# Kernel optimization log

Hardware: AMD Instinct MI355X
Metric: run time of the kernel (lower is better)

Reference implementation:

```python
import jax, jax.numpy as jnp
import numpy as np

M, A, H, T = 6, 4096, 128, 30   # num_modes, num_actors, hidden_size, future_steps
HIST = 50
MAX_T = 6.0
DT = MAX_T / T                   # min_stepsize: one Euler step per prediction interval
MIN_SCALE = 0.001
EPS = 1e-5

def _ln(x, g, b):
    mu = x.mean(-1, keepdims=True)
    v = ((x - mu) ** 2).mean(-1, keepdims=True)
    return (x - mu) * jax.lax.rsqrt(v + EPS) * g + b

def setup_inputs() -> dict:
    key = jax.random.key(0)
    ks = iter(jax.random.split(key, 64))
    def p(shape):
        return jax.random.normal(next(ks), shape, jnp.float32) * 0.02
    inp = {
        'local_embed':  jax.random.normal(next(ks), (A, H), jnp.float32),
        'global_embed': jax.random.normal(next(ks), (M, A, H), jnp.float32),
        'noise':        jax.random.normal(next(ks), (T, M * A, H), jnp.float32),
        # aggr_embed: Linear(2H,H) + LayerNorm
        'aggr_w': p((2 * H, H)), 'aggr_b': p((H,)),
        'aggr_g': jnp.ones((H,), jnp.float32), 'aggr_be': jnp.zeros((H,), jnp.float32),
        # FFunc (posterior drift): Linear(H+2,H)-Tanh-Linear(H,H)-Tanh-Linear(H,H)
        'f_w1': p((H + 2, H)), 'f_b1': p((H,)),
        'f_w2': p((H, H)),     'f_b2': p((H,)),
        'f_w3': p((H, H)),     'f_b3': p((H,)),
        # GFunc (diffusion): Linear(H+2,H)-Tanh-Linear(H,H)-Tanh-Linear(H,1)-Sigmoid
        'g_w1': p((H + 2, H)), 'g_b1': p((H,)),
        'g_w2': p((H, H)),     'g_b2': p((H,)),
        'g_w3': p((H, 1)),     'g_b3': p((1,)),
        # decoder: Linear(H,H)+LN+ReLU+Linear(H,2)
        'd_w1': p((H, H)), 'd_b1': p((H,)),
        'd_g': jnp.ones((H,), jnp.float32), 'd_be': jnp.zeros((H,), jnp.float32),
        'd_w2': p((H, 2)), 'd_b2': p((2,)),
        # scale head (uncertain=True): same structure as decoder
        's_w1': p((H, H)), 's_b1': p((H,)),
        's_g': jnp.ones((H,), jnp.float32), 's_be': jnp.zeros((H,), jnp.float32),
        's_w2': p((H, 2)), 's_b2': p((2,)),
        # pi head: Linear(2H,H)+LN+ReLU+Linear(H,1)
        'p_w1': p((2 * H, H)), 'p_b1': p((H,)),
        'p_g': jnp.ones((H,), jnp.float32), 'p_be': jnp.zeros((H,), jnp.float32),
        'p_w2': p((H, 1)), 'p_b2': p((1,)),
        'padding_mask': jnp.zeros((A, HIST), dtype=bool),
    }
    return inp

def reference(local_embed, global_embed, noise,
              aggr_w, aggr_b, aggr_g, aggr_be,
              f_w1, f_b1, f_w2, f_b2, f_w3, f_b3,
              g_w1, g_b1, g_w2, g_b2, g_w3, g_b3,
              d_w1, d_b1, d_g, d_be, d_w2, d_b2,
              s_w1, s_b1, s_g, s_be, s_w2, s_b2,
              p_w1, p_b1, p_g, p_be, p_w2, p_b2,
              padding_mask):
    N = M * A
    le = jnp.broadcast_to(local_embed, (M, A, H))
    # aggr_embed(cat(global, local))
    x = jnp.concatenate([global_embed, le], axis=-1)
    h0 = jax.nn.relu(_ln(x @ aggr_w + aggr_b, aggr_g, aggr_be)).reshape(N, H)

    def with_time(y, t):
        tc = jnp.ones((y.shape[0], 1), y.dtype) * t
        return jnp.concatenate([y, jnp.sin(tc), jnp.cos(tc)], axis=-1)

    def drift(t, y):  # FFunc
        i = with_time(y, t)
        h = jnp.tanh(i @ f_w1 + f_b1)
        h = jnp.tanh(h @ f_w2 + f_b2)
        return h @ f_w3 + f_b3

    def diffusion(t, y):  # GFunc -> scalar per sample, repeated over dims
        i = with_time(y, t)
        h = jnp.tanh(i @ g_w1 + g_b1)
        h = jnp.tanh(h @ g_w2 + g_b2)
        return jax.nn.sigmoid(h @ g_w3 + g_b3)  # [N,1]

    ts = jnp.linspace(0.0, MAX_T, T + 1)[:-1]  # left endpoints of each Euler step
    sqdt = jnp.sqrt(jnp.asarray(DT, h0.dtype))

    def step(y, tz):
        t, z = tz
        y2 = y + drift(t, y) * DT + diffusion(t, y) * sqdt * z
        return y2, y2

    _, ys = jax.lax.scan(step, h0, (ts, noise))  # [T, N, H]
    sol_y = ys.transpose(1, 0, 2)                # [N, T, H]

    dh = jax.nn.relu(_ln(sol_y @ d_w1 + d_b1, d_g, d_be))
    loc = (dh @ d_w2 + d_b2).reshape(M, A, T, 2)
    sh = jax.nn.relu(_ln(sol_y @ s_w1 + s_b1, s_g, s_be))
    scale = jax.nn.elu(sh @ s_w2 + s_b2) + 1.0 + MIN_SCALE
    scale = scale.reshape(M, A, T, 2)
    loc_out = jnp.concatenate([loc, scale], axis=-1)  # [M, A, T, 4]

    pin = jnp.concatenate([le, global_embed], axis=-1)
    pi = (jax.nn.relu(_ln(pin @ p_w1 + p_b1, p_g, p_be)) @ p_w2 + p_b2)
    pi = pi.squeeze(-1).T                              # [A, M]

    reg_mask = ~padding_mask[:, -T:]
    return loc_out, pi, reg_mask
```

## Files before the change

kernel.cpp:

```cpp
#include <hip/hip_runtime.h>

#define Adim 4096
#define HD 128
#define TSTEPS 30
#define NROWS 24576
#define RBLK 32
#define NBLKS 768
#define DT_C 0.2f
#define SQDT_C 0.44721359549995794f
#define LN_EPS 1e-5f

#define PI_OFF   2949120
#define MASK_OFF 2973696

typedef unsigned short u16;
typedef __bf16 bf16x8 __attribute__((ext_vector_type(8)));
typedef float f32x4 __attribute__((ext_vector_type(4)));

__device__ __forceinline__ u16 f2bf(float x){
    unsigned u = __builtin_bit_cast(unsigned, x);
    u = (u + 0x7fffu + ((u >> 16) & 1u)) >> 16;
    return (u16)u;
}
__device__ __forceinline__ float bf2f(unsigned h){
    unsigned u = (h & 0xffffu) << 16;
    return __builtin_bit_cast(float, u);
}
__device__ __forceinline__ unsigned pack2(float a, float b){
    unsigned r;
    asm("v_cvt_pk_bf16_f32 %0, %1, %2" : "=v"(r) : "v"(a), "v"(b));
    return r;
}
__device__ __forceinline__ float tanh_f(float x){
    return 1.0f - 2.0f / (1.0f + __expf(2.0f * x));
}
__device__ __forceinline__ float sigm_f(float x){
    return 1.0f / (1.0f + __expf(-x));
}
#define SWZ(r,k) ((k) ^ (((r)&7)<<3))

#define MFMA(A,B,C) __builtin_amdgcn_mfma_f32_16x16x32_bf16(A, B, C, 0, 0, 0)

__device__ __forceinline__ void loadW(const u16* __restrict__ img, int lane, int wid,
                                      bf16x8 W[4]) {
    const int c = wid*16 + (lane & 15);
    const int kq = lane >> 4;
#pragma unroll
    for (int kk = 0; kk < 4; ++kk)
        W[kk] = *reinterpret_cast<const bf16x8*>(img + c*HD + SWZ(c, kk*32 + kq*8));
}

__device__ __forceinline__ void gemm1(const u16* __restrict__ act, const bf16x8 (&W)[4],
                                      int lane, f32x4 acc[2]) {
    const int rl = lane & 15, kq = lane >> 4;
#pragma unroll
    for (int tr = 0; tr < 2; ++tr) {
        const int r = tr*16 + rl;
        const u16* arow = act + r*HD;
        f32x4 a = {0.f,0.f,0.f,0.f};
#pragma unroll
        for (int kk = 0; kk < 4; ++kk) {
            bf16x8 bf = *reinterpret_cast<const bf16x8*>(arow + SWZ(r, kk*32 + kq*8));
            a = MFMA(W[kk], bf, a);
        }
        acc[tr] = a;
    }
}
__device__ __forceinline__ void gemm2(const u16* __restrict__ act,
                                      const bf16x8 (&Wx)[4], const bf16x8 (&Wy)[4],
                                      int lane, f32x4 accX[2], f32x4 accY[2]) {
    const int rl = lane & 15, kq = lane >> 4;
#pragma unroll
    for (int tr = 0; tr < 2; ++tr) {
        const int r = tr*16 + rl;
        const u16* arow = act + r*HD;
        f32x4 ax = {0.f,0.f,0.f,0.f}, ay = {0.f,0.f,0.f,0.f};
#pragma unroll
        for (int kk = 0; kk < 4; ++kk) {
            bf16x8 bf = *reinterpret_cast<const bf16x8*>(arow + SWZ(r, kk*32 + kq*8));
            ax = MFMA(Wx[kk], bf, ax);
            ay = MFMA(Wy[kk], bf, ay);
        }
        accX[tr] = ax; accY[tr] = ay;
    }
}
__device__ __forceinline__ void gemm4(const u16* __restrict__ act,
                                      const bf16x8 (&W1)[4], const bf16x8 (&W2)[4],
                                      const bf16x8 (&W3)[4], const bf16x8 (&W4)[4],
                                      int lane, f32x4 a1[2], f32x4 a2[2],
                                      f32x4 a3[2], f32x4 a4[2]) {
    const int rl = lane & 15, kq = lane >> 4;
#pragma unroll
    for (int tr = 0; tr < 2; ++tr) {
        const int r = tr*16 + rl;
        const u16* arow = act + r*HD;
        f32x4 x1={0.f,0.f,0.f,0.f}, x2={0.f,0.f,0.f,0.f};
        f32x4 x3={0.f,0.f,0.f,0.f}, x4={0.f,0.f,0.f,0.f};
#pragma unroll
        for (int kk = 0; kk < 4; ++kk) {
            bf16x8 bf = *reinterpret_cast<const bf16x8*>(arow + SWZ(r, kk*32 + kq*8));
            x1 = MFMA(W1[kk], bf, x1);
            x2 = MFMA(W2[kk], bf, x2);
            x3 = MFMA(W3[kk], bf, x3);
            x4 = MFMA(W4[kk], bf, x4);
        }
        a1[tr]=x1; a2[tr]=x2; a3[tr]=x3; a4[tr]=x4;
    }
}

__device__ __forceinline__ void epiT(const f32x4 acc[2], const float b[4],
                                     u16* dst, int lane, int wid) {
    const int c0 = wid*16 + ((lane>>4)<<2);
    const int rl = lane & 15;
#pragma unroll
    for (int tr = 0; tr < 2; ++tr) {
        int r = tr*16 + rl;
        float v0 = tanh_f(acc[tr][0] + b[0]);
        float v1 = tanh_f(acc[tr][1] + b[1]);
        float v2 = tanh_f(acc[tr][2] + b[2]);
        float v3 = tanh_f(acc[tr][3] + b[3]);
        uint2 pk = { pack2(v0, v1), pack2(v2, v3) };
        *reinterpret_cast<uint2*>(dst + r*HD + SWZ(r, c0)) = pk;
    }
}
__device__ __forceinline__ void epiN(const f32x4 acc[2], const float b[4],
                                     u16* dst, int lane, int wid) {
    const int c0 = wid*16 + ((lane>>4)<<2);
    const int rl = lane & 15;
#pragma unroll
    for (int tr = 0; tr < 2; ++tr) {
        int r = tr*16 + rl;
        uint2 pk = { pack2(acc[tr][0]+b[0], acc[tr][1]+b[1]),
                     pack2(acc[tr][2]+b[2], acc[tr][3]+b[3]) };
        *reinterpret_cast<uint2*>(dst + r*HD + SWZ(r, c0)) = pk;
    }
}
__device__ __forceinline__ void epiF(const f32x4 acc[2], const float* __restrict__ bias,
                                     float* dst, int lane, int wid) {
    const int c0 = wid*16 + ((lane>>4)<<2);
    const int rl = lane & 15;
    float4 b4 = *reinterpret_cast<const float4*>(bias + c0);
#pragma unroll
    for (int tr = 0; tr < 2; ++tr) {
        int r = tr*16 + rl;
        float4 v = { acc[tr][0]+b4.x, acc[tr][1]+b4.y, acc[tr][2]+b4.z, acc[tr][3]+b4.w };
        *reinterpret_cast<float4*>(dst + r*HD + c0) = v;
    }
}

__device__ __forceinline__ void gemmX(const u16* __restrict__ Xc, int kBase,
                                      const u16* __restrict__ img,
                                      int lane, int wid, f32x4 acc[2], bool init) {
    bf16x8 W[4]; loadW(img, lane, wid, W);
    const int rl = lane & 15, kq = lane >> 4;
#pragma unroll
    for (int tr = 0; tr < 2; ++tr) {
        const int r = tr*16 + rl;
        const u16* arow = Xc + r*256;
        f32x4 a = init ? f32x4{0.f,0.f,0.f,0.f} : acc[tr];
#pragma unroll
        for (int kk = 0; kk < 4; ++kk) {
            bf16x8 bf = *reinterpret_cast<const bf16x8*>(arow + SWZ(r, kBase + kk*32 + kq*8));
            a = MFMA(W[kk], bf, a);
        }
        acc[tr] = a;
    }
}

__device__ __forceinline__ void head_ln(const u16* __restrict__ src,
                                        const float4* __restrict__ pp4,
                                        float b20, float b21, int elu, int off, int idx,
                                        float* __restrict__ outStage)
{
    int row = idx >> 3, sub = idx & 7;
    int c0 = sub * 16;
    uint4 p0 = *reinterpret_cast<const uint4*>(src + row*HD + SWZ(row, c0));
    uint4 p1 = *reinterpret_cast<const uint4*>(src + row*HD + SWZ(row, c0+8));
    float v[16];
    v[0]=bf2f(p0.x); v[1]=bf2f(p0.x>>16); v[2]=bf2f(p0.y); v[3]=bf2f(p0.y>>16);
    v[4]=bf2f(p0.z); v[5]=bf2f(p0.z>>16); v[6]=bf2f(p0.w); v[7]=bf2f(p0.w>>16);
    v[8]=bf2f(p1.x); v[9]=bf2f(p1.x>>16); v[10]=bf2f(p1.y); v[11]=bf2f(p1.y>>16);
    v[12]=bf2f(p1.z); v[13]=bf2f(p1.z>>16); v[14]=bf2f(p1.w); v[15]=bf2f(p1.w>>16);
    float s = 0.f, sq = 0.f;
#pragma unroll
    for (int i = 0; i < 16; ++i){ s += v[i]; sq += v[i]*v[i]; }
    s += __shfl_xor(s,1); sq += __shfl_xor(sq,1);
    s += __shfl_xor(s,2); sq += __shfl_xor(sq,2);
    s += __shfl_xor(s,4); sq += __shfl_xor(sq,4);
    float mu = s * (1.f/128.f);
    float rstd = rsqrtf(sq*(1.f/128.f) - mu*mu + LN_EPS);
    float a0 = 0.f, a1 = 0.f;
#pragma unroll
    for (int i = 0; i < 16; ++i){
        float4 p = pp4[(c0 + i) ^ sub];
        float h = (v[i]-mu)*rstd*p.x + p.y;
        h = fmaxf(h, 0.f);
        a0 += h * p.z; a1 += h * p.w;
    }
    a0 += __shfl_xor(a0,1); a1 += __shfl_xor(a1,1);
    a0 += __shfl_xor(a0,2); a1 += __shfl_xor(a1,2);
    a0 += __shfl_xor(a0,4); a1 += __shfl_xor(a1,4);
    if (sub == 0){
        a0 += b20; a1 += b21;
        if (elu){
            a0 = (a0 > 0.f ? a0 : __expf(a0)-1.f) + 1.001f;
            a1 = (a1 > 0.f ? a1 : __expf(a1)-1.f) + 1.001f;
        }
        outStage[row*4 + off]   = a0;
        outStage[row*4 + off+1] = a1;
    }
}

__global__ void prep_w(const float* __restrict__ fw1, const float* __restrict__ fw2,
                       const float* __restrict__ fw3, const float* __restrict__ gw1,
                       const float* __restrict__ gw2, const float* __restrict__ dw1,
                       const float* __restrict__ sw1, const float* __restrict__ aw,
                       const float* __restrict__ pw1, u16* __restrict__ ws)
{
    int img = blockIdx.y;
    int idx = blockIdx.x * 256 + threadIdx.x;
    int k = idx >> 7, j = idx & 127;
    const float* W = fw1; int sr = k;
    switch (img) {
        case 0: W = fw1; break;  case 1: W = fw2; break;  case 2: W = fw3; break;
        case 3: W = gw1; break;  case 4: W = gw2; break;
        case 5: W = dw1; break;  case 6: W = sw1; break;
        case 7: W = aw;  break;  case 8: W = aw;  sr = k + 128; break;
        case 9: W = pw1; break;  case 10: W = pw1; sr = k + 128; break;
    }
    ws[(size_t)img*16384 + j*128 + SWZ(j, k)] = f2bf(W[(size_t)sr*128 + j]);
}

__global__ void reorder_out(const float* __restrict__ wsOut, float* __restrict__ outp)
{
    __shared__ float tile[3840];
    int b = blockIdx.x;
    const float* src = wsOut + (size_t)b*3840;
#pragma unroll
    for (int j = 0; j < 15; ++j) {
        int idx = j*256 + threadIdx.x;
        int tt = idx >> 7, rc = idx & 127;
        int row = rc >> 2, c = idx & 3;
        tile[row*120 + tt*4 + c] = src[idx];
    }
    __syncthreads();
    float* dst = outp + (size_t)b*3840;
#pragma unroll
    for (int j = 0; j < 15; ++j) {
        int idx = j*256 + threadIdx.x;
        dst[idx] = tile[idx];
    }
}

__global__ __launch_bounds__(512, 2) void sde_fused(
    const float* __restrict__ lE, const float* __restrict__ gE,
    const float* __restrict__ noise,
    const float* __restrict__ aggr_b, const float* __restrict__ aggr_g, const float* __restrict__ aggr_be,
    const float* __restrict__ fw1, const float* __restrict__ fb1,
    const float* __restrict__ fb2, const float* __restrict__ fb3,
    const float* __restrict__ gw1, const float* __restrict__ gb1,
    const float* __restrict__ gb2, const float* __restrict__ gw3, const float* __restrict__ gb3,
    const float* __restrict__ db1, const float* __restrict__ dg, const float* __restrict__ dbe,
    const float* __restrict__ dw2, const float* __restrict__ db2,
    const float* __restrict__ sb1, const float* __restrict__ sg, const float* __restrict__ sbe,
    const float* __restrict__ sw2, const float* __restrict__ sb2,
    const float* __restrict__ pb1, const float* __restrict__ pg, const float* __restrict__ pbe,
    const float* __restrict__ pw2, const float* __restrict__ pb2,
    const unsigned char* __restrict__ pmask,
    const u16* __restrict__ wimg,
    float* __restrict__ wsOut,
    float* __restrict__ outp)
{
    __shared__ __align__(16) unsigned char SMEM[61952];
    u16*  Sb    = (u16*)SMEM;
    u16*  Ab    = (u16*)(SMEM + 8192);
    u16*  Bb    = (u16*)(SMEM + 16384);
    u16*  Cb    = (u16*)(SMEM + 24576);
    u16*  Fb    = (u16*)(SMEM + 32768);
    u16*  Db    = (u16*)(SMEM + 40960);
    u16*  Eb    = (u16*)(SMEM + 49152);
    float4* ppd = (float4*)(SMEM + 57344);
    float4* pps = (float4*)(SMEM + 59392);
    float* outStage = (float*)(SMEM + 61440);
    u16*  Xc    = (u16*)(SMEM + 40960);
    float* preLN = (float*)(SMEM + 8192);

    const int tid  = threadIdx.x;
    const int lane = tid & 63;
    const int wid  = tid >> 6;
    const int bid  = blockIdx.x;
    const int r0   = bid * RBLK;
    const int c0e  = wid*16 + ((lane>>4)<<2);

    if (tid < 128) {
        int cs = tid ^ ((tid >> 4) & 7);
        ppd[cs] = make_float4(dg[tid], dbe[tid], dw2[2*tid], dw2[2*tid+1]);
        pps[cs] = make_float4(sg[tid], sbe[tid], sw2[2*tid], sw2[2*tid+1]);
    }
#pragma unroll
    for (int i = 0; i < 2; ++i) {
        int gidx = i*512 + tid;
        int r = gidx >> 5;
        int k = (gidx & 31) * 8;
        int gr = r0 + r;
        const float* src = (k < HD) ? (gE + (size_t)gr*HD + k)
                                    : (lE + (size_t)(gr & (Adim-1))*HD + (k - HD));
        float4 v0 = reinterpret_cast<const float4*>(src)[0];
        float4 v1 = reinterpret_cast<const float4*>(src)[1];
        uint4 pk = { pack2(v0.x, v0.y), pack2(v0.z, v0.w),
                     pack2(v1.x, v1.y), pack2(v1.z, v1.w) };
        *reinterpret_cast<uint4*>(Xc + r*256 + SWZ(r, k)) = pk;
    }
    __syncthreads();

    f32x4 acc[2];

    gemmX(Xc, 0,   wimg + 10*16384, lane, wid, acc, true);
    gemmX(Xc, 128, wimg + 9*16384,  lane, wid, acc, false);
    epiF(acc, pb1, preLN, lane, wid);
    __syncthreads();
    {
        int row = tid >> 4, sub = tid & 15;
        int c0 = sub * 8;
        const float* yr = preLN + row*HD + c0;
        float v[8]; float s = 0.f, sq = 0.f;
#pragma unroll
        for (int i = 0; i < 8; ++i){ float x = yr[i]; v[i] = x; s += x; sq += x*x; }
        s += __shfl_xor(s,1); sq += __shfl_xor(sq,1);
        s += __shfl_xor(s,2); sq += __shfl_xor(sq,2);
        s += __shfl_xor(s,4); sq += __shfl_xor(sq,4);
        s += __shfl_xor(s,8); sq += __shfl_xor(sq,8);
        float mu = s*(1.f/128.f);
        float rstd = rsqrtf(sq*(1.f/128.f) - mu*mu + LN_EPS);
        float a0 = 0.f;
#pragma unroll
        for (int i = 0; i < 8; ++i){
            int cc = c0 + i;
            float h = (v[i]-mu)*rstd*pg[cc] + pbe[cc];
            a0 += fmaxf(h, 0.f) * pw2[cc];
        }
        a0 += __shfl_xor(a0,1); a0 += __shfl_xor(a0,2);
        a0 += __shfl_xor(a0,4); a0 += __shfl_xor(a0,8);
        if (sub == 0) {
            int gr = r0 + row;
            outp[PI_OFF + (size_t)(gr & (Adim-1))*6 + (gr >> 12)] = a0 + pb2[0];
        }
    }
    if (tid < RBLK) {
        int gr = r0 + tid;
        if (gr < Adim) {
            const unsigned char* pm = pmask + (size_t)gr*50 + 20;
            float* o = outp + MASK_OFF + (size_t)gr*TSTEPS;
#pragma unroll
            for (int i = 0; i < TSTEPS; ++i) o[i] = pm[i] ? 0.f : 1.f;
        }
    }
    __syncthreads();

    gemmX(Xc, 0,   wimg + 7*16384, lane, wid, acc, true);
    gemmX(Xc, 128, wimg + 8*16384, lane, wid, acc, false);
    __syncthreads();
    epiF(acc, aggr_b, preLN, lane, wid);
    __syncthreads();

    float y0,y1,y2,y3,y4,y5,y6,y7;
    {
        int row = tid >> 4, sub = tid & 15;
        int c0 = sub * 8;
        const float* yr = preLN + row*HD + c0;
        float v[8]; float s = 0.f, sq = 0.f;
#pragma unroll
        for (int i = 0; i < 8; ++i){ float x = yr[i]; v[i] = x; s += x; sq += x*x; }
        s += __shfl_xor(s,1); sq += __shfl_xor(sq,1);
        s += __shfl_xor(s,2); sq += __shfl_xor(sq,2);
        s += __shfl_xor(s,4); sq += __shfl_xor(sq,4);
        s += __shfl_xor(s,8); sq += __shfl_xor(sq,8);
        float mu = s*(1.f/128.f);
        float rstd = rsqrtf(sq*(1.f/128.f) - mu*mu + LN_EPS);
#pragma unroll
        for (int i = 0; i < 8; ++i){
            int cc = c0 + i;
            float h = (v[i]-mu)*rstd*aggr_g[cc] + aggr_be[cc];
            v[i] = fmaxf(h, 0.f);
        }
        y0=v[0]; y1=v[1]; y2=v[2]; y3=v[3]; y4=v[4]; y5=v[5]; y6=v[6]; y7=v[7];
        uint4 pk = { pack2(v[0],v[1]), pack2(v[2],v[3]),
                     pack2(v[4],v[5]), pack2(v[6],v[7]) };
        *reinterpret_cast<uint4*>(&Sb[row*HD + SWZ(row, c0)]) = pk;
    }

    bf16x8 WF1[4], WG1[4], WF2[4], WG2[4], WF3[4], WD1[4], WS1[4];
    loadW(wimg + 0*16384, lane, wid, WF1);
    loadW(wimg + 3*16384, lane, wid, WG1);
    loadW(wimg + 1*16384, lane, wid, WF2);
    loadW(wimg + 4*16384, lane, wid, WG2);
    loadW(wimg + 2*16384, lane, wid, WF3);
    loadW(wimg + 5*16384, lane, wid, WD1);
    loadW(wimg + 6*16384, lane, wid, WS1);

    float fb2c[4], gb2c[4], fb3c[4], db1c[4], sb1c[4];
    float fb1c[4], gb1c[4], fw1s[4], fw1cc[4], gw1s[4], gw1cc[4];
#pragma unroll
    for (int q = 0; q < 4; ++q) {
        int c = c0e + q;
        fb2c[q]=fb2[c]; gb2c[q]=gb2[c]; fb3c[q]=fb3[c]; db1c[q]=db1[c]; sb1c[q]=sb1[c];
        fb1c[q]=fb1[c]; gb1c[q]=gb1[c];
        fw1s[q]=fw1[128*HD+c]; fw1cc[q]=fw1[129*HD+c];
        gw1s[q]=gw1[128*HD+c]; gw1cc[q]=gw1[129*HD+c];
    }
    float g3r[8];
#pragma unroll
    for (int j = 0; j < 8; ++j) g3r[j] = gw3[(tid & 15)*8 + j];
    const float db20 = db2[0], db21 = db2[1];
    const float sb20 = sb2[0], sb21 = sb2[1];
    const float gb3v = gb3[0];

    float4 nz0, nz1;
    __syncthreads();

    {
        float bF[4], bG[4];
#pragma unroll
        for (int q = 0; q < 4; ++q) { bF[q] = fb1c[q] + fw1cc[q]; bG[q] = gb1c[q] + gw1cc[q]; }
        f32x4 aF[2], aG[2];
        gemm2(Sb, WF1, WG1, lane, aF, aG);
        epiT(aF, bF, Ab, lane, wid);
        epiT(aG, bG, Bb, lane, wid);
        const float* np = noise + ((size_t)r0)*HD + (size_t)tid*8;
        nz0 = reinterpret_cast<const float4*>(np)[0];
        nz1 = reinterpret_cast<const float4*>(np)[1];
    }
    __syncthreads();

    for (int k = 0; k < TSTEPS; ++k) {
        {
            f32x4 a1[2];
            gemm1(Ab, WF2, lane, a1);
            epiT(a1, fb2c, Cb, lane, wid);
            gemm1(Bb, WG2, lane, a1);
            epiT(a1, gb2c, Fb, lane, wid);
        }
        if (k) {
            if (tid < 256) head_ln(Db, ppd, db20, db21, 0, 0, tid, outStage);
            else           head_ln(Eb, pps, sb20, sb21, 1, 2, tid-256, outStage);
        }
        __syncthreads();
        {
            f32x4 a1[2];
            gemm1(Cb, WF3, lane, a1);
            epiN(a1, fb3c, Db, lane, wid);
        }
        float growv;
        {
            int row = tid >> 4, sub = tid & 15;
            uint4 pk = *reinterpret_cast<const uint4*>(Fb + row*HD + SWZ(row, sub*8));
            float s = bf2f(pk.x)*g3r[0] + bf2f(pk.x>>16)*g3r[1]
                    + bf2f(pk.y)*g3r[2] + bf2f(pk.y>>16)*g3r[3]
                    + bf2f(pk.z)*g3r[4] + bf2f(pk.z>>16)*g3r[5]
                    + bf2f(pk.w)*g3r[6] + bf2f(pk.w>>16)*g3r[7];
            s += __shfl_xor(s,1); s += __shfl_xor(s,2);
            s += __shfl_xor(s,4); s += __shfl_xor(s,8);
            growv = sigm_f(s + gb3v);
        }
        __syncthreads();
        {
            int row = tid >> 4, sub = tid & 15;
            int sk = SWZ(row, sub*8);
            uint4 dpk = *reinterpret_cast<const uint4*>(Db + row*HD + sk);
            float g = growv * SQDT_C;
            y0 += bf2f(dpk.x)     * DT_C + g*nz0.x;
            y1 += bf2f(dpk.x>>16) * DT_C + g*nz0.y;
            y2 += bf2f(dpk.y)     * DT_C + g*nz0.z;
            y3 += bf2f(dpk.y>>16) * DT_C + g*nz0.w;
            y4 += bf2f(dpk.z)     * DT_C + g*nz1.x;
            y5 += bf2f(dpk.z>>16) * DT_C + g*nz1.y;
            y6 += bf2f(dpk.w)     * DT_C + g*nz1.z;
            y7 += bf2f(dpk.w>>16) * DT_C + g*nz1.w;
            uint4 s4 = { pack2(y0,y1), pack2(y2,y3), pack2(y4,y5), pack2(y6,y7) };
            *reinterpret_cast<uint4*>(Sb + row*HD + sk) = s4;
        }
        __syncthreads();
        if (k < TSTEPS-1) {
            float t = (k+1) * DT_C;
            float st = __sinf(t), ct = __cosf(t);
            float bF[4], bG[4];
#pragma unroll
            for (int q = 0; q < 4; ++q) {
                bF[q] = fb1c[q] + st*fw1s[q] + ct*fw1cc[q];
                bG[q] = gb1c[q] + st*gw1s[q] + ct*gw1cc[q];
            }
            f32x4 aF[2], aG[2], aD[2], aS[2];
            gemm4(Sb, WF1, WG1, WD1, WS1, lane, aF, aG, aD, aS);
            epiT(aF, bF, Ab, lane, wid);
            epiT(aG, bG, Bb, lane, wid);
            epiN(aD, db1c, Db, lane, wid);
            epiN(aS, sb1c, Eb, lane, wid);
            const float* np = noise + ((size_t)(k+1)*NROWS + r0)*HD + (size_t)tid*8;
            nz0 = reinterpret_cast<const float4*>(np)[0];
            nz1 = reinterpret_cast<const float4*>(np)[1];
            if (k >= 1 && tid < 128)
                wsOut[((size_t)bid*TSTEPS + (k-1))*128 + tid] = outStage[tid];
        } else {
            f32x4 aD[2], aS[2];
            gemm2(Sb, WD1, WS1, lane, aD, aS);
            epiN(aD, db1c, Db, lane, wid);
            epiN(aS, sb1c, Eb, lane, wid);
            if (tid < 128)
                wsOut[((size_t)bid*TSTEPS + (TSTEPS-2))*128 + tid] = outStage[tid];
        }
        __syncthreads();
    }
    if (tid < 256) head_ln(Db, ppd, db20, db21, 0, 0, tid, outStage);
    else           head_ln(Eb, pps, sb20, sb21, 1, 2, tid-256, outStage);
    __syncthreads();
    if (tid < 128)
        wsOut[((size_t)bid*TSTEPS + (TSTEPS-1))*128 + tid] = outStage[tid];
}

extern "C" void kernel_launch(void* const* d_in, const int* in_sizes, int n_in,
                              void* d_out, int out_size, void* d_ws, size_t ws_size,
                              hipStream_t stream) {
    const float* lE      = (const float*)d_in[0];
    const float* gE      = (const float*)d_in[1];
    const float* noise   = (const float*)d_in[2];
    const float* aggr_w  = (const float*)d_in[3];
    const float* aggr_b  = (const float*)d_in[4];
    const float* aggr_g  = (const float*)d_in[5];
    const float* aggr_be = (const float*)d_in[6];
    const float* fw1 = (const float*)d_in[7];
    const float* fb1 = (const float*)d_in[8];
    const float* fw2 = (const float*)d_in[9];
    const float* fb2 = (const float*)d_in[10];
    const float* fw3 = (const float*)d_in[11];
    const float* fb3 = (const float*)d_in[12];
    const float* gw1 = (const float*)d_in[13];
    const float* gb1 = (const float*)d_in[14];
    const float* gw2 = (const float*)d_in[15];
    const float* gb2 = (const float*)d_in[16];
    const float* gw3 = (const float*)d_in[17];
    const float* gb3 = (const float*)d_in[18];
    const float* dw1 = (const float*)d_in[19];
    const float* db1 = (const float*)d_in[20];
    const float* dg  = (const float*)d_in[21];
    const float* dbe = (const float*)d_in[22];
    const float* dw2 = (const float*)d_in[23];
    const float* db2 = (const float*)d_in[24];
    const float* sw1 = (const float*)d_in[25];
    const float* sb1 = (const float*)d_in[26];
    const float* sg  = (const float*)d_in[27];
    const float* sbe = (const float*)d_in[28];
    const float* sw2 = (const float*)d_in[29];
    const float* sb2 = (const float*)d_in[30];
    const float* pw1 = (const float*)d_in[31];
    const float* pb1 = (const float*)d_in[32];
    const float* pg  = (const float*)d_in[33];
    const float* pbe = (const float*)d_in[34];
    const float* pw2 = (const float*)d_in[35];
    const float* pb2 = (const float*)d_in[36];
    const unsigned char* pmask = (const unsigned char*)d_in[37];
    float* outp = (float*)d_out;
    u16* wimg = (u16*)d_ws;
    float* wsOut = (float*)((char*)d_ws + 360448);

    prep_w<<<dim3(64, 11), 256, 0, stream>>>(fw1, fw2, fw3, gw1, gw2, dw1, sw1,
                                             aggr_w, pw1, wimg);
    sde_fused<<<NBLKS, 512, 0, stream>>>(
        lE, gE, noise, aggr_b, aggr_g, aggr_be,
        fw1, fb1, fb2, fb3,
        gw1, gb1, gb2, gw3, gb3,
        db1, dg, dbe, dw2, db2,
        sb1, sg, sbe, sw2, sb2,
        pb1, pg, pbe, pw2, pb2,
        pmask, wimg, wsOut, outp);
    reorder_out<<<NBLKS, 256, 0, stream>>>(wsOut, outp);
}
```

Before: 593.5 us.

## Interleave three 32-row sub-tiles per block in a staggered phase pipeline

```diff
diff --git a/kernel.cpp b/kernel.cpp
--- a/kernel.cpp
+++ b/kernel.cpp
@@ -4,8 +4,8 @@
 #define HD 128
 #define TSTEPS 30
 #define NROWS 24576
-#define RBLK 32
-#define NBLKS 768
+#define RBLK 96
+#define NBLKS 256
 #define DT_C 0.2f
 #define SQDT_C 0.44721359549995794f
 #define LN_EPS 1e-5f
@@ -38,7 +38,6 @@
     return 1.0f / (1.0f + __expf(-x));
 }
 #define SWZ(r,k) ((k) ^ (((r)&7)<<3))
-
 #define MFMA(A,B,C) __builtin_amdgcn_mfma_f32_16x16x32_bf16(A, B, C, 0, 0, 0)
 
 __device__ __forceinline__ void loadW(const u16* __restrict__ img, int lane, int wid,
@@ -209,6 +208,228 @@
         outStage[row*4 + off]   = a0;
         outStage[row*4 + off+1] = a1;
     }
+}
+
+__device__ __forceinline__ void ph0x(int st, const u16* Sb, u16* Ab, u16* Bb,
+    u16* Db, u16* Eb, const float* biasT, int lane, int wid, int c0e,
+    const bf16x8 (&WF1)[4], const bf16x8 (&WG1)[4],
+    const bf16x8 (&WD1)[4], const bf16x8 (&WS1)[4])
+{
+    const bool doL1 = (st < TSTEPS), doDS = (st >= 1);
+    float bF[4], bG[4], bD[4], bS[4];
+    if (doL1) {
+        float tt = st * DT_C;
+        float sn = __sinf(tt), cn = __cosf(tt);
+        float4 a0 = *(const float4*)(biasT + 0*128 + c0e);
+        float4 a1 = *(const float4*)(biasT + 1*128 + c0e);
+        float4 a2 = *(const float4*)(biasT + 2*128 + c0e);
+        float4 a3 = *(const float4*)(biasT + 3*128 + c0e);
+        float4 a4 = *(const float4*)(biasT + 4*128 + c0e);
+        float4 a5 = *(const float4*)(biasT + 5*128 + c0e);
+#pragma unroll
+        for (int q = 0; q < 4; ++q) {
+            bF[q] = ((const float*)&a0)[q] + sn*((const float*)&a1)[q] + cn*((const float*)&a2)[q];
+            bG[q] = ((const float*)&a3)[q] + sn*((const float*)&a4)[q] + cn*((const float*)&a5)[q];
+        }
+    }
+    if (doDS) {
+        float4 a9 = *(const float4*)(biasT + 9*128 + c0e);
+        float4 aa = *(const float4*)(biasT + 10*128 + c0e);
+#pragma unroll
+        for (int q = 0; q < 4; ++q) { bD[q]=((const float*)&a9)[q]; bS[q]=((const float*)&aa)[q]; }
+    }
+    if (doL1 && doDS) {
+        f32x4 aF[2], aG[2], aD[2], aS[2];
+        gemm4(Sb, WF1, WG1, WD1, WS1, lane, aF, aG, aD, aS);
+        epiT(aF, bF, Ab, lane, wid);
+        epiT(aG, bG, Bb, lane, wid);
+        epiN(aD, bD, Db, lane, wid);
+        epiN(aS, bS, Eb, lane, wid);
+    } else if (doL1) {
+        f32x4 aF[2], aG[2];
+        gemm2(Sb, WF1, WG1, lane, aF, aG);
+        epiT(aF, bF, Ab, lane, wid);
+        epiT(aG, bG, Bb, lane, wid);
+    } else if (doDS) {
+        f32x4 aD[2], aS[2];
+        gemm2(Sb, WD1, WS1, lane, aD, aS);
+        epiN(aD, bD, Db, lane, wid);
+        epiN(aS, bS, Eb, lane, wid);
+    }
+}
+
+__device__ __forceinline__ void ph1x(int st, const u16* Ab, const u16* Bb, u16* Cb,
+    const u16* Db, const u16* Eb, float* gpw, float* outS,
+    const float4* ppd, const float4* pps, const float* biasT,
+    int tid, int lane, int wid, int c0e,
+    float db20, float db21, float sb20, float sb21,
+    const bf16x8 (&WF2)[4], const bf16x8 (&WG2)[4])
+{
+    if (st < TSTEPS) {
+        float4 b6 = *(const float4*)(biasT + 6*128 + c0e);
+        float bb[4] = { b6.x, b6.y, b6.z, b6.w };
+        f32x4 a1[2];
+        gemm1(Ab, WF2, lane, a1);
+        epiT(a1, bb, Cb, lane, wid);
+        float4 b7 = *(const float4*)(biasT + 7*128 + c0e);
+        float4 g3 = *(const float4*)(biasT + 11*128 + c0e);
+        gemm1(Bb, WG2, lane, a1);
+        float p0 = tanh_f(a1[0][0]+b7.x)*g3.x + tanh_f(a1[0][1]+b7.y)*g3.y
+                 + tanh_f(a1[0][2]+b7.z)*g3.z + tanh_f(a1[0][3]+b7.w)*g3.w;
+        float p1 = tanh_f(a1[1][0]+b7.x)*g3.x + tanh_f(a1[1][1]+b7.y)*g3.y
+                 + tanh_f(a1[1][2]+b7.z)*g3.z + tanh_f(a1[1][3]+b7.w)*g3.w;
+        p0 += __shfl_xor(p0, 16); p0 += __shfl_xor(p0, 32);
+        p1 += __shfl_xor(p1, 16); p1 += __shfl_xor(p1, 32);
+        if ((lane >> 4) == 0) {
+            int rl2 = lane & 15;
+            gpw[rl2*9 + wid]      = p0;
+            gpw[(16+rl2)*9 + wid] = p1;
+        }
+    }
+    if (st >= 1) {
+        if (tid < 256) head_ln(Db, ppd, db20, db21, 0, 0, tid, outS);
+        else           head_ln(Eb, pps, sb20, sb21, 1, 2, tid-256, outS);
+    }
+}
+
+__device__ __forceinline__ void ph2x(int st, const u16* Cb, u16* Db,
+    const float* gpr, const float* biasT, const float* __restrict__ nbase,
+    float* __restrict__ wsb, const float* outS,
+    int tid, int lane, int wid, int c0e, float gb3v,
+    float4& nz0, float4& nz1, float& grow, const bf16x8 (&WF3)[4])
+{
+    if (st < TSTEPS) {
+        const float* np = nbase + (size_t)st*NROWS*HD + (size_t)tid*8;
+        nz0 = reinterpret_cast<const float4*>(np)[0];
+        nz1 = reinterpret_cast<const float4*>(np)[1];
+        float4 b8 = *(const float4*)(biasT + 8*128 + c0e);
+        float bb[4] = { b8.x, b8.y, b8.z, b8.w };
+        f32x4 a1[2];
+        gemm1(Cb, WF3, lane, a1);
+        epiN(a1, bb, Db, lane, wid);
+        int row = tid >> 4, sub = tid & 15;
+        float s = (sub < 8) ? gpr[row*9 + sub] : 0.f;
+        s += __shfl_xor(s,1); s += __shfl_xor(s,2);
+        s += __shfl_xor(s,4); s += __shfl_xor(s,8);
+        grow = sigm_f(s + gb3v) * SQDT_C;
+    }
+    if (st >= 1 && tid < 128)
+        wsb[(size_t)(st-1)*128 + tid] = outS[tid];
+}
+
+__device__ __forceinline__ void ph3x(int st, const u16* Db, u16* Sb, int tid,
+    float (&y)[8], const float4& nz0, const float4& nz1, float grow)
+{
+    if (st >= TSTEPS) return;
+    int row = tid >> 4, k0 = (tid & 15)*8, sk = SWZ(row, k0);
+    uint4 dpk = *reinterpret_cast<const uint4*>(Db + row*HD + sk);
+    y[0] += bf2f(dpk.x)     * DT_C + grow*nz0.x;
+    y[1] += bf2f(dpk.x>>16) * DT_C + grow*nz0.y;
+    y[2] += bf2f(dpk.y)     * DT_C + grow*nz0.z;
+    y[3] += bf2f(dpk.y>>16) * DT_C + grow*nz0.w;
+    y[4] += bf2f(dpk.z)     * DT_C + grow*nz1.x;
+    y[5] += bf2f(dpk.z>>16) * DT_C + grow*nz1.y;
+    y[6] += bf2f(dpk.w)     * DT_C + grow*nz1.z;
+    y[7] += bf2f(dpk.w>>16) * DT_C + grow*nz1.w;
+    uint4 s4 = { pack2(y[0],y[1]), pack2(y[2],y[3]), pack2(y[4],y[5]), pack2(y[6],y[7]) };
+    *reinterpret_cast<uint4*>(Sb + row*HD + sk) = s4;
+}
+
+__device__ __forceinline__ void prologueB(int rb0, u16* Xc, float* preLN, u16* Sb,
+    const float* lE, const float* gE,
+    const float* aggr_b, const float* aggr_g, const float* aggr_be,
+    const float* pb1, const float* pg, const float* pbe,
+    const float* pw2, const float* pb2,
+    const unsigned char* pmask, const u16* wimg, float* outp,
+    int tid, int lane, int wid, float (&y)[8])
+{
+#pragma unroll
+    for (int i = 0; i < 2; ++i) {
+        int gidx = i*512 + tid;
+        int r = gidx >> 5;
+        int k = (gidx & 31) * 8;
+        int gr = rb0 + r;
+        const float* src = (k < HD) ? (gE + (size_t)gr*HD + k)
+                                    : (lE + (size_t)(gr & (Adim-1))*HD + (k - HD));
+        float4 v0 = reinterpret_cast<const float4*>(src)[0];
+        float4 v1 = reinterpret_cast<const float4*>(src)[1];
+        uint4 pk = { pack2(v0.x, v0.y), pack2(v0.z, v0.w),
+                     pack2(v1.x, v1.y), pack2(v1.z, v1.w) };
+        *reinterpret_cast<uint4*>(Xc + r*256 + SWZ(r, k)) = pk;
+    }
+    __syncthreads();
+    f32x4 acc[2];
+    gemmX(Xc, 0,   wimg + 10*16384, lane, wid, acc, true);
+    gemmX(Xc, 128, wimg + 9*16384,  lane, wid, acc, false);
+    epiF(acc, pb1, preLN, lane, wid);
+    __syncthreads();
+    {
+        int row = tid >> 4, sub = tid & 15;
+        int c0 = sub * 8;
+        const float* yr = preLN + row*HD + c0;
+        float v[8]; float s = 0.f, sq = 0.f;
+#pragma unroll
+        for (int i = 0; i < 8; ++i){ float x = yr[i]; v[i] = x; s += x; sq += x*x; }
+        s += __shfl_xor(s,1); sq += __shfl_xor(sq,1);
+        s += __shfl_xor(s,2); sq += __shfl_xor(sq,2);
+        s += __shfl_xor(s,4); sq += __shfl_xor(sq,4);
+        s += __shfl_xor(s,8); sq += __shfl_xor(sq,8);
+        float mu = s*(1.f/128.f);
+        float rstd = rsqrtf(sq*(1.f/128.f) - mu*mu + LN_EPS);
+        float a0 = 0.f;
+#pragma unroll
+        for (int i = 0; i < 8; ++i){
+            int cc = c0 + i;
+            float h = (v[i]-mu)*rstd*pg[cc] + pbe[cc];
+            a0 += fmaxf(h, 0.f) * pw2[cc];
+        }
+        a0 += __shfl_xor(a0,1); a0 += __shfl_xor(a0,2);
+        a0 += __shfl_xor(a0,4); a0 += __shfl_xor(a0,8);
+        if (sub == 0) {
+            int gr = rb0 + row;
+            outp[PI_OFF + (size_t)(gr & (Adim-1))*6 + (gr >> 12)] = a0 + pb2[0];
+        }
+    }
+    if (tid < 32) {
+        int gr = rb0 + tid;
+        if (gr < Adim) {
+            const unsigned char* pm = pmask + (size_t)gr*50 + 20;
+            float* o = outp + MASK_OFF + (size_t)gr*TSTEPS;
+#pragma unroll
+            for (int i = 0; i < TSTEPS; ++i) o[i] = pm[i] ? 0.f : 1.f;
+        }
+    }
+    __syncthreads();
+    gemmX(Xc, 0,   wimg + 7*16384, lane, wid, acc, true);
+    gemmX(Xc, 128, wimg + 8*16384, lane, wid, acc, false);
+    epiF(acc, aggr_b, preLN, lane, wid);
+    __syncthreads();
+    {
+        int row = tid >> 4, sub = tid & 15;
+        int c0 = sub * 8;
+        const float* yr = preLN + row*HD + c0;
+        float v[8]; float s = 0.f, sq = 0.f;
+#pragma unroll
+        for (int i = 0; i < 8; ++i){ float x = yr[i]; v[i] = x; s += x; sq += x*x; }
+        s += __shfl_xor(s,1); sq += __shfl_xor(sq,1);
+        s += __shfl_xor(s,2); sq += __shfl_xor(sq,2);
+        s += __shfl_xor(s,4); sq += __shfl_xor(sq,4);
+        s += __shfl_xor(s,8); sq += __shfl_xor(sq,8);
+        float mu = s*(1.f/128.f);
+        float rstd = rsqrtf(sq*(1.f/128.f) - mu*mu + LN_EPS);
+#pragma unroll
+        for (int i = 0; i < 8; ++i){
+            int cc = c0 + i;
+            float h = (v[i]-mu)*rstd*aggr_g[cc] + aggr_be[cc];
+            v[i] = fmaxf(h, 0.f);
+        }
+#pragma unroll
+        for (int i = 0; i < 8; ++i) y[i] = v[i];
+        uint4 pk = { pack2(v[0],v[1]), pack2(v[2],v[3]),
+                     pack2(v[4],v[5]), pack2(v[6],v[7]) };
+        *reinterpret_cast<uint4*>(&Sb[row*HD + SWZ(row, c0)]) = pk;
+    }
+    __syncthreads();
 }
 
 __global__ void prep_w(const float* __restrict__ fw1, const float* __restrict__ fw2,
@@ -271,19 +492,23 @@
     float* __restrict__ wsOut,
     float* __restrict__ outp)
 {
-    __shared__ __align__(16) unsigned char SMEM[61952];
-    u16*  Sb    = (u16*)SMEM;
-    u16*  Ab    = (u16*)(SMEM + 8192);
-    u16*  Bb    = (u16*)(SMEM + 16384);
-    u16*  Cb    = (u16*)(SMEM + 24576);
-    u16*  Fb    = (u16*)(SMEM + 32768);
-    u16*  Db    = (u16*)(SMEM + 40960);
-    u16*  Eb    = (u16*)(SMEM + 49152);
-    float4* ppd = (float4*)(SMEM + 57344);
-    float4* pps = (float4*)(SMEM + 59392);
-    float* outStage = (float*)(SMEM + 61440);
-    u16*  Xc    = (u16*)(SMEM + 40960);
-    float* preLN = (float*)(SMEM + 8192);
+    __shared__ __align__(16) unsigned char SMEM[161536];
+    u16* Sb0 = (u16*)(SMEM +      0); u16* Ab0 = (u16*)(SMEM +  8192);
+    u16* Bb0 = (u16*)(SMEM +  16384); u16* Cb0 = (u16*)(SMEM + 24576);
+    u16* Db0 = (u16*)(SMEM +  32768); u16* Eb0 = (u16*)(SMEM + 40960);
+    u16* Sb1 = (u16*)(SMEM +  49152); u16* Ab1 = (u16*)(SMEM + 57344);
+    u16* Bb1 = (u16*)(SMEM +  65536); u16* Cb1 = (u16*)(SMEM + 73728);
+    u16* Db1 = (u16*)(SMEM +  81920); u16* Eb1 = (u16*)(SMEM + 90112);
+    u16* Sb2 = (u16*)(SMEM +  98304); u16* Ab2 = (u16*)(SMEM + 106496);
+    u16* Bb2 = (u16*)(SMEM + 114688); u16* Cb2 = (u16*)(SMEM + 122880);
+    u16* Db2 = (u16*)(SMEM + 131072); u16* Eb2 = (u16*)(SMEM + 139264);
+    float* gpart = (float*)(SMEM + 147456);
+    float* biasT = (float*)(SMEM + 149760);
+    float4* ppd  = (float4*)(SMEM + 155904);
+    float4* pps  = (float4*)(SMEM + 157952);
+    float* outS0 = (float*)(SMEM + 160000);
+    float* outS1 = (float*)(SMEM + 160512);
+    float* outS2 = (float*)(SMEM + 161024);
 
     const int tid  = threadIdx.x;
     const int lane = tid & 63;
@@ -296,98 +521,27 @@
         int cs = tid ^ ((tid >> 4) & 7);
         ppd[cs] = make_float4(dg[tid], dbe[tid], dw2[2*tid], dw2[2*tid+1]);
         pps[cs] = make_float4(sg[tid], sbe[tid], sw2[2*tid], sw2[2*tid+1]);
-    }
-#pragma unroll
-    for (int i = 0; i < 2; ++i) {
-        int gidx = i*512 + tid;
-        int r = gidx >> 5;
-        int k = (gidx & 31) * 8;
-        int gr = r0 + r;
-        const float* src = (k < HD) ? (gE + (size_t)gr*HD + k)
-                                    : (lE + (size_t)(gr & (Adim-1))*HD + (k - HD));
-        float4 v0 = reinterpret_cast<const float4*>(src)[0];
-        float4 v1 = reinterpret_cast<const float4*>(src)[1];
-        uint4 pk = { pack2(v0.x, v0.y), pack2(v0.z, v0.w),
-                     pack2(v1.x, v1.y), pack2(v1.z, v1.w) };
-        *reinterpret_cast<uint4*>(Xc + r*256 + SWZ(r, k)) = pk;
-    }
-    __syncthreads();
-
-    f32x4 acc[2];
-
-    gemmX(Xc, 0,   wimg + 10*16384, lane, wid, acc, true);
-    gemmX(Xc, 128, wimg + 9*16384,  lane, wid, acc, false);
-    epiF(acc, pb1, preLN, lane, wid);
-    __syncthreads();
-    {
-        int row = tid >> 4, sub = tid & 15;
-        int c0 = sub * 8;
-        const float* yr = preLN + row*HD + c0;
-        float v[8]; float s = 0.f, sq = 0.f;
-#pragma unroll
-        for (int i = 0; i < 8; ++i){ float x = yr[i]; v[i] = x; s += x; sq += x*x; }
-        s += __shfl_xor(s,1); sq += __shfl_xor(sq,1);
-        s += __shfl_xor(s,2); sq += __shfl_xor(sq,2);
-        s += __shfl_xor(s,4); sq += __shfl_xor(sq,4);
-        s += __shfl_xor(s,8); sq += __shfl_xor(sq,8);
-        float mu = s*(1.f/128.f);
-        float rstd = rsqrtf(sq*(1.f/128.f) - mu*mu + LN_EPS);
-        float a0 = 0.f;
-#pragma unroll
-        for (int i = 0; i < 8; ++i){
-            int cc = c0 + i;
-            float h = (v[i]-mu)*rstd*pg[cc] + pbe[cc];
-            a0 += fmaxf(h, 0.f) * pw2[cc];
-        }
-        a0 += __shfl_xor(a0,1); a0 += __shfl_xor(a0,2);
-        a0 += __shfl_xor(a0,4); a0 += __shfl_xor(a0,8);
-        if (sub == 0) {
-            int gr = r0 + row;
-            outp[PI_OFF + (size_t)(gr & (Adim-1))*6 + (gr >> 12)] = a0 + pb2[0];
-        }
-    }
-    if (tid < RBLK) {
-        int gr = r0 + tid;
-        if (gr < Adim) {
-            const unsigned char* pm = pmask + (size_t)gr*50 + 20;
-            float* o = outp + MASK_OFF + (size_t)gr*TSTEPS;
-#pragma unroll
-            for (int i = 0; i < TSTEPS; ++i) o[i] = pm[i] ? 0.f : 1.f;
-        }
-    }
-    __syncthreads();
-
-    gemmX(Xc, 0,   wimg + 7*16384, lane, wid, acc, true);
-    gemmX(Xc, 128, wimg + 8*16384, lane, wid, acc, false);
-    __syncthreads();
-    epiF(acc, aggr_b, preLN, lane, wid);
-    __syncthreads();
-
-    float y0,y1,y2,y3,y4,y5,y6,y7;
-    {
-        int row = tid >> 4, sub = tid & 15;
-        int c0 = sub * 8;
-        const float* yr = preLN + row*HD + c0;
-        float v[8]; float s = 0.f, sq = 0.f;
-#pragma unroll
-        for (int i = 0; i < 8; ++i){ float x = yr[i]; v[i] = x; s += x; sq += x*x; }
-        s += __shfl_xor(s,1); sq += __shfl_xor(sq,1);
-        s += __shfl_xor(s,2); sq += __shfl_xor(sq,2);
-        s += __shfl_xor(s,4); sq += __shfl_xor(sq,4);
-        s += __shfl_xor(s,8); sq += __shfl_xor(sq,8);
-        float mu = s*(1.f/128.f);
-        float rstd = rsqrtf(sq*(1.f/128.f) - mu*mu + LN_EPS);
-#pragma unroll
-        for (int i = 0; i < 8; ++i){
-            int cc = c0 + i;
-            float h = (v[i]-mu)*rstd*aggr_g[cc] + aggr_be[cc];
-            v[i] = fmaxf(h, 0.f);
-        }
-        y0=v[0]; y1=v[1]; y2=v[2]; y3=v[3]; y4=v[4]; y5=v[5]; y6=v[6]; y7=v[7];
-        uint4 pk = { pack2(v[0],v[1]), pack2(v[2],v[3]),
-                     pack2(v[4],v[5]), pack2(v[6],v[7]) };
-        *reinterpret_cast<uint4*>(&Sb[row*HD + SWZ(row, c0)]) = pk;
-    }
+        biasT[0*128+tid]  = fb1[tid];
+        biasT[1*128+tid]  = fw1[128*HD+tid];
+        biasT[2*128+tid]  = fw1[129*HD+tid];
+        biasT[3*128+tid]  = gb1[tid];
+        biasT[4*128+tid]  = gw1[128*HD+tid];
+        biasT[5*128+tid]  = gw1[129*HD+tid];
+        biasT[6*128+tid]  = fb2[tid];
+        biasT[7*128+tid]  = gb2[tid];
+        biasT[8*128+tid]  = fb3[tid];
+        biasT[9*128+tid]  = db1[tid];
+        biasT[10*128+tid] = sb1[tid];
+        biasT[11*128+tid] = gw3[tid];
+    }
+
+    float y0[8], y1[8], y2[8];
+    prologueB(r0,    Ab0, (float*)Cb0, Sb0, lE, gE, aggr_b, aggr_g, aggr_be,
+              pb1, pg, pbe, pw2, pb2, pmask, wimg, outp, tid, lane, wid, y0);
+    prologueB(r0+32, Ab1, (float*)Cb1, Sb1, lE, gE, aggr_b, aggr_g, aggr_be,
+              pb1, pg, pbe, pw2, pb2, pmask, wimg, outp, tid, lane, wid, y1);
+    prologueB(r0+64, Ab2, (float*)Cb2, Sb2, lE, gE, aggr_b, aggr_g, aggr_be,
+              pb1, pg, pbe, pw2, pb2, pmask, wimg, outp, tid, lane, wid, y2);
 
     bf16x8 WF1[4], WG1[4], WF2[4], WG2[4], WF3[4], WD1[4], WS1[4];
     loadW(wimg + 0*16384, lane, wid, WF1);
@@ -398,123 +552,63 @@
     loadW(wimg + 5*16384, lane, wid, WD1);
     loadW(wimg + 6*16384, lane, wid, WS1);
 
-    float fb2c[4], gb2c[4], fb3c[4], db1c[4], sb1c[4];
-    float fb1c[4], gb1c[4], fw1s[4], fw1cc[4], gw1s[4], gw1cc[4];
-#pragma unroll
-    for (int q = 0; q < 4; ++q) {
-        int c = c0e + q;
-        fb2c[q]=fb2[c]; gb2c[q]=gb2[c]; fb3c[q]=fb3[c]; db1c[q]=db1[c]; sb1c[q]=sb1[c];
-        fb1c[q]=fb1[c]; gb1c[q]=gb1[c];
-        fw1s[q]=fw1[128*HD+c]; fw1cc[q]=fw1[129*HD+c];
-        gw1s[q]=gw1[128*HD+c]; gw1cc[q]=gw1[129*HD+c];
-    }
-    float g3r[8];
-#pragma unroll
-    for (int j = 0; j < 8; ++j) g3r[j] = gw3[(tid & 15)*8 + j];
     const float db20 = db2[0], db21 = db2[1];
     const float sb20 = sb2[0], sb21 = sb2[1];
     const float gb3v = gb3[0];
 
-    float4 nz0, nz1;
+    const float* nb0 = noise + (size_t)(r0     )*HD;
+    const float* nb1 = noise + (size_t)(r0 + 32)*HD;
+    const float* nb2 = noise + (size_t)(r0 + 64)*HD;
+    float* ws0 = wsOut + (size_t)(bid*3 + 0)*TSTEPS*128;
+    float* ws1 = wsOut + (size_t)(bid*3 + 1)*TSTEPS*128;
+    float* ws2 = wsOut + (size_t)(bid*3 + 2)*TSTEPS*128;
+
+    float4 nA0, nA1, nB0, nB1, nC0, nC1;
+    float gA = 0.f, gB = 0.f, gC = 0.f;
+
     __syncthreads();
 
-    {
-        float bF[4], bG[4];
-#pragma unroll
-        for (int q = 0; q < 4; ++q) { bF[q] = fb1c[q] + fw1cc[q]; bG[q] = gb1c[q] + gw1cc[q]; }
-        f32x4 aF[2], aG[2];
-        gemm2(Sb, WF1, WG1, lane, aF, aG);
-        epiT(aF, bF, Ab, lane, wid);
-        epiT(aG, bG, Bb, lane, wid);
-        const float* np = noise + ((size_t)r0)*HD + (size_t)tid*8;
-        nz0 = reinterpret_cast<const float4*>(np)[0];
-        nz1 = reinterpret_cast<const float4*>(np)[1];
-    }
-    __syncthreads();
-
-    for (int k = 0; k < TSTEPS; ++k) {
+    const int TMAX = 4*TSTEPS + 2;
+    for (int iv = 0; iv <= 4*TSTEPS + 4; ++iv) {
+        const int par = iv & 1, rpar = par ^ 1;
         {
-            f32x4 a1[2];
-            gemm1(Ab, WF2, lane, a1);
-            epiT(a1, fb2c, Cb, lane, wid);
-            gemm1(Bb, WG2, lane, a1);
-            epiT(a1, gb2c, Fb, lane, wid);
-        }
-        if (k) {
-            if (tid < 256) head_ln(Db, ppd, db20, db21, 0, 0, tid, outStage);
-            else           head_ln(Eb, pps, sb20, sb21, 1, 2, tid-256, outStage);
+            int t = iv;
+            if (t <= TMAX) {
+                int ph = t & 3, st = t >> 2;
+                if      (ph == 0) ph0x(st, Sb0, Ab0, Bb0, Db0, Eb0, biasT, lane, wid, c0e, WF1, WG1, WD1, WS1);
+                else if (ph == 1) ph1x(st, Ab0, Bb0, Cb0, Db0, Eb0, gpart + par*288, outS0,
+                                       ppd, pps, biasT, tid, lane, wid, c0e, db20, db21, sb20, sb21, WF2, WG2);
+                else if (ph == 2) ph2x(st, Cb0, Db0, gpart + rpar*288, biasT, nb0, ws0, outS0,
+                                       tid, lane, wid, c0e, gb3v, nA0, nA1, gA, WF3);
+                else              ph3x(st, Db0, Sb0, tid, y0, nA0, nA1, gA);
+            }
+        }
+        {
+            int t = iv - 1;
+            if (t >= 0 && t <= TMAX) {
+                int ph = t & 3, st = t >> 2;
+                if      (ph == 0) ph0x(st, Sb1, Ab1, Bb1, Db1, Eb1, biasT, lane, wid, c0e, WF1, WG1, WD1, WS1);
+                else if (ph == 1) ph1x(st, Ab1, Bb1, Cb1, Db1, Eb1, gpart + par*288, outS1,
+                                       ppd, pps, biasT, tid, lane, wid, c0e, db20, db21, sb20, sb21, WF2, WG2);
+                else if (ph == 2) ph2x(st, Cb1, Db1, gpart + rpar*288, biasT, nb1, ws1, outS1,
+                                       tid, lane, wid, c0e, gb3v, nB0, nB1, gB, WF3);
+                else              ph3x(st, Db1, Sb1, tid, y1, nB0, nB1, gB);
+            }
+        }
+        {
+            int t = iv - 2;
+            if (t >= 0 && t <= TMAX) {
+                int ph = t & 3, st = t >> 2;
+                if      (ph == 0) ph0x(st, Sb2, Ab2, Bb2, Db2, Eb2, biasT, lane, wid, c0e, WF1, WG1, WD1, WS1);
+                else if (ph == 1) ph1x(st, Ab2, Bb2, Cb2, Db2, Eb2, gpart + par*288, outS2,
+                                       ppd, pps, biasT, tid, lane, wid, c0e, db20, db21, sb20, sb21, WF2, WG2);
+                else if (ph == 2) ph2x(st, Cb2, Db2, gpart + rpar*288, biasT, nb2, ws2, outS2,
+                                       tid, lane, wid, c0e, gb3v, nC0, nC1, gC, WF3);
+                else              ph3x(st, Db2, Sb2, tid, y2, nC0, nC1, gC);
+            }
         }
         __syncthreads();
-        {
-            f32x4 a1[2];
-            gemm1(Cb, WF3, lane, a1);
-            epiN(a1, fb3c, Db, lane, wid);
-        }
-        float growv;
-        {
-            int row = tid >> 4, sub = tid & 15;
-            uint4 pk = *reinterpret_cast<const uint4*>(Fb + row*HD + SWZ(row, sub*8));
-            float s = bf2f(pk.x)*g3r[0] + bf2f(pk.x>>16)*g3r[1]
-                    + bf2f(pk.y)*g3r[2] + bf2f(pk.y>>16)*g3r[3]
-                    + bf2f(pk.z)*g3r[4] + bf2f(pk.z>>16)*g3r[5]
-                    + bf2f(pk.w)*g3r[6] + bf2f(pk.w>>16)*g3r[7];
-            s += __shfl_xor(s,1); s += __shfl_xor(s,2);
-            s += __shfl_xor(s,4); s += __shfl_xor(s,8);
-            growv = sigm_f(s + gb3v);
-        }
-        __syncthreads();
-        {
-            int row = tid >> 4, sub = tid & 15;
-            int sk = SWZ(row, sub*8);
-            uint4 dpk = *reinterpret_cast<const uint4*>(Db + row*HD + sk);
-            float g = growv * SQDT_C;
-            y0 += bf2f(dpk.x)     * DT_C + g*nz0.x;
-            y1 += bf2f(dpk.x>>16) * DT_C + g*nz0.y;
-            y2 += bf2f(dpk.y)     * DT_C + g*nz0.z;
-            y3 += bf2f(dpk.y>>16) * DT_C + g*nz0.w;
-            y4 += bf2f(dpk.z)     * DT_C + g*nz1.x;
-            y5 += bf2f(dpk.z>>16) * DT_C + g*nz1.y;
-            y6 += bf2f(dpk.w)     * DT_C + g*nz1.z;
-            y7 += bf2f(dpk.w>>16) * DT_C + g*nz1.w;
-            uint4 s4 = { pack2(y0,y1), pack2(y2,y3), pack2(y4,y5), pack2(y6,y7) };
-            *reinterpret_cast<uint4*>(Sb + row*HD + sk) = s4;
-        }
-        __syncthreads();
-        if (k < TSTEPS-1) {
-            float t = (k+1) * DT_C;
-            float st = __sinf(t), ct = __cosf(t);
-            float bF[4], bG[4];
-#pragma unroll
-            for (int q = 0; q < 4; ++q) {
-                bF[q] = fb1c[q] + st*fw1s[q] + ct*fw1cc[q];
-                bG[q] = gb1c[q] + st*gw1s[q] + ct*gw1cc[q];
-            }
-            f32x4 aF[2], aG[2], aD[2], aS[2];
-            gemm4(Sb, WF1, WG1, WD1, WS1, lane, aF, aG, aD, aS);
-            epiT(aF, bF, Ab, lane, wid);
-            epiT(aG, bG, Bb, lane, wid);
-            epiN(aD, db1c, Db, lane, wid);
-            epiN(aS, sb1c, Eb, lane, wid);
-            const float* np = noise + ((size_t)(k+1)*NROWS + r0)*HD + (size_t)tid*8;
-            nz0 = reinterpret_cast<const float4*>(np)[0];
-            nz1 = reinterpret_cast<const float4*>(np)[1];
-            if (k >= 1 && tid < 128)
-                wsOut[((size_t)bid*TSTEPS + (k-1))*128 + tid] = outStage[tid];
-        } else {
-            f32x4 aD[2], aS[2];
-            gemm2(Sb, WD1, WS1, lane, aD, aS);
-            epiN(aD, db1c, Db, lane, wid);
-            epiN(aS, sb1c, Eb, lane, wid);
-            if (tid < 128)
-                wsOut[((size_t)bid*TSTEPS + (TSTEPS-2))*128 + tid] = outStage[tid];
-        }
-        __syncthreads();
-    }
-    if (tid < 256) head_ln(Db, ppd, db20, db21, 0, 0, tid, outStage);
-    else           head_ln(Eb, pps, sb20, sb21, 1, 2, tid-256, outStage);
-    __syncthreads();
-    if (tid < 128)
-        wsOut[((size_t)bid*TSTEPS + (TSTEPS-1))*128 + tid] = outStage[tid];
+    }
 }
 
 extern "C" void kernel_launch(void* const* d_in, const int* in_sizes, int n_in,
@@ -572,5 +666,5 @@
         sb1, sg, sbe, sw2, sb2,
         pb1, pg, pbe, pw2, pb2,
         pmask, wimg, wsOut, outp);
-    reorder_out<<<NBLKS, 256, 0, stream>>>(wsOut, outp);
-}
+    reorder_out<<<768, 256, 0, stream>>>(wsOut, outp);
+}
```

Measured after the change: 879.9 us. +48.3%, slower.
